# Kernel optimization log

Measured on AMD Instinct MI355X. Metric: run time of the kernel, lower is better.

Reference implementation:

```python
import jax, jax.numpy as jnp
import numpy as np

NUM_ANCHORS = 9


def select_tensor(tensor, inds):
    # tensor: (b, 9*c, h, w) -> rows (b*h*w*9, c), gather at inds (faithful to source layout)
    bs, c9, h, w = tensor.shape
    c = c9 // NUM_ANCHORS
    t = tensor.reshape(bs, NUM_ANCHORS, c, h * w).transpose(0, 3, 1, 2).reshape(-1, c)
    return t[inds]


def bilinear_sample(feat, bidx, ys, xs):
    # feat: (b, c, H, W); bidx/ys/xs: (P,). torchvision-style: 0 outside [-1, H]x[-1, W].
    H, W = feat.shape[2], feat.shape[3]
    invalid = (ys < -1.0) | (ys > H) | (xs < -1.0) | (xs > W)
    y = jnp.clip(ys, 0.0, H - 1)
    x = jnp.clip(xs, 0.0, W - 1)
    y0 = jnp.floor(y).astype(jnp.int32)
    x0 = jnp.floor(x).astype(jnp.int32)
    y1 = jnp.minimum(y0 + 1, H - 1)
    x1 = jnp.minimum(x0 + 1, W - 1)
    ly = (y - y0)[:, None]
    lx = (x - x0)[:, None]
    hy = 1.0 - ly
    hx = 1.0 - lx
    v00 = feat[bidx, :, y0, x0]
    v01 = feat[bidx, :, y0, x1]
    v10 = feat[bidx, :, y1, x0]
    v11 = feat[bidx, :, y1, x1]
    out = hy * hx * v00 + hy * lx * v01 + ly * hx * v10 + ly * lx * v11
    return jnp.where(invalid[:, None], 0.0, out)


def roi_align_3x3(feat, boxes, batch_idx):
    # output_size=(3,3), spatial_scale=1, sampling_ratio=1 (one center sample/bin), aligned=False
    OUT = 3
    n = boxes.shape[0]
    x1, y1, x2, y2 = boxes[:, 0], boxes[:, 1], boxes[:, 2], boxes[:, 3]
    roi_w = jnp.maximum(x2 - x1, 1.0)
    roi_h = jnp.maximum(y2 - y1, 1.0)
    bw = roi_w / OUT
    bh = roi_h / OUT
    g = jnp.arange(OUT, dtype=jnp.float32) + 0.5
    ys = jnp.broadcast_to(y1[:, None, None] + g[None, :, None] * bh[:, None, None], (n, OUT, OUT)).reshape(-1)
    xs = jnp.broadcast_to(x1[:, None, None] + g[None, None, :] * bw[:, None, None], (n, OUT, OUT)).reshape(-1)
    bidx = jnp.repeat(batch_idx, OUT * OUT)
    vals = bilinear_sample(feat, bidx, ys, xs)  # (n*9, c)
    return vals.reshape(n, OUT, OUT, feat.shape[1]).transpose(0, 3, 1, 2)  # (n, c, 3, 3)


def setup_inputs() -> dict:
    key = jax.random.key(0)
    ks = jax.random.split(key, 8)
    b, c, h, w = 8, 256, 128, 128
    return {
        "feat": jax.random.normal(ks[0], (b, c, h, w), dtype=jnp.float32),
        "hm": jax.random.uniform(ks[1], (b, 9, h, w), dtype=jnp.float32),
        "wh": jax.random.normal(ks[2], (b, 36, h, w), dtype=jnp.float32) * 4.0,
        "offset": jax.random.normal(ks[3], (b, 18, h, w), dtype=jnp.float32),
        "w_fc1": jax.random.normal(ks[4], (c * 9, 1024), dtype=jnp.float32) * 0.02,
        "b_fc1": jnp.zeros((1024,), dtype=jnp.float32),
        "w_cls": jax.random.normal(ks[5], (1024, 10), dtype=jnp.float32) * 0.02,
        "b_cls": jnp.zeros((10,), dtype=jnp.float32),
        "w_wh": jax.random.normal(ks[6], (1024, 4), dtype=jnp.float32) * 0.02,
        "b_wh": jnp.zeros((4,), dtype=jnp.float32),
        "k": 100,
    }


def reference(feat, hm, wh, offset, w_fc1, b_fc1, w_cls, b_cls, w_wh, b_wh, k):
    bs, _, h, w_ = hm.shape
    hw = h * w_
    # get_inds (inds=None path): topk over (b, h*w*9) with (h, w, anchor) flat layout
    flat = hm.transpose(0, 2, 3, 1).reshape(bs, -1)
    top_v, top_i = jax.lax.top_k(flat, k)
    value = top_v.reshape(-1)
    top_i = top_i.reshape(-1)
    stage1_cls = top_i % NUM_ANCHORS
    pos = (top_i // NUM_ANCHORS) % hw
    inds = pos + jnp.repeat(jnp.arange(bs, dtype=top_i.dtype) * hw, k)
    # select_tensor gathers (stage1 and for_stage2 use the same inds in the inference path)
    wh_sel = select_tensor(wh, inds)       # (b*k, 4)
    off_sel = select_tensor(offset, inds)  # (b*k, 2)
    # box arithmetic (faithful: ys = inds // w keeps the batch offset, as in the source)
    xs = (inds % w_).astype(jnp.float32) + off_sel[:, 0]
    ys = (inds // w_).astype(jnp.float32) + off_sel[:, 1]
    batch_idx = jnp.repeat(jnp.arange(bs), k)
    boxes = jnp.stack([xs + wh_sel[:, 0], ys + wh_sel[:, 1],
                       xs + wh_sel[:, 2], ys + wh_sel[:, 3]], axis=1)
    roi_feat = roi_align_3x3(feat, boxes, batch_idx)  # (b*k, c, 3, 3)
    # stage 2 head
    hdn = jax.nn.relu(roi_feat.reshape(roi_feat.shape[0], -1) @ w_fc1 + b_fc1)
    stage2_cls = hdn @ w_cls + b_cls
    stage2_wh = hdn @ w_wh + b_wh
    return (hm, wh_sel, off_sel, stage1_cls, wh_sel, off_sel, stage2_cls, stage2_wh, inds, value)
```

## Files before the change

### kernel.cpp

```cpp
#include <hip/hip_runtime.h>
#include <hip/hip_bf16.h>
#include <stdint.h>

#define HW      16384
#define W_      128
#define NA      9
#define BS      8
#define K_TOP   100
#define NDET    800
#define MPAD    832
#define C_FEAT  256
#define FC1_IN  2304
#define FC1_OUT 1024

#define O_HM    0
#define O_WH1   1179648
#define O_OFF1  1182848
#define O_S1CLS 1184448
#define O_WH2   1185248
#define O_OFF2  1188448
#define O_CLS   1190048
#define O_SWH   1198048
#define O_INDS  1201248
#define O_VAL   1202048

#define NBIN     1024
#define CAND_MAX 512
#define HBLK     36

typedef __attribute__((ext_vector_type(8))) short short8v;
typedef __attribute__((ext_vector_type(4))) float f32x4;

__device__ __forceinline__ void gload16(const void* g, void* l) {
    __builtin_amdgcn_global_load_lds(
        (const __attribute__((address_space(1))) unsigned int*)g,
        (__attribute__((address_space(3))) unsigned int*)l, 16, 0, 0);
}

__device__ __forceinline__ int binof(float v) {
    return max(0, min(NBIN - 1, (int)(v * (float)NBIN)));
}

__global__ __launch_bounds__(256) void hist_kernel(const float* __restrict__ hm,
                                                   float* __restrict__ out,
                                                   unsigned int* __restrict__ hist) {
    const int tid = threadIdx.x;
    const int b = blockIdx.x / HBLK, sub = blockIdx.x % HBLK;
    __shared__ unsigned int lh[NBIN];
    for (int i = tid; i < NBIN; i += 256) lh[i] = 0u;
    __syncthreads();
    const float4* src = (const float4*)(hm + (size_t)b * NA * HW) + sub * 1024;
    float4*       dst = (float4*)(out + O_HM + (size_t)b * NA * HW) + sub * 1024;
    #pragma unroll
    for (int t = 0; t < 4; ++t) {
        float4 v = src[t * 256 + tid];
        dst[t * 256 + tid] = v;
        atomicAdd(&lh[binof(v.x)], 1u);
        atomicAdd(&lh[binof(v.y)], 1u);
        atomicAdd(&lh[binof(v.z)], 1u);
        atomicAdd(&lh[binof(v.w)], 1u);
    }
    __syncthreads();
    for (int i = tid; i < NBIN; i += 256)
        if (lh[i]) atomicAdd(&hist[b * NBIN + i], lh[i]);
}

__global__ __launch_bounds__(512) void thresh_kernel(const unsigned int* __restrict__ hist,
                                                     int* __restrict__ thr) {
    const int b = threadIdx.x >> 6, lane = threadIdx.x & 63;
    const unsigned int* h = hist + b * NBIN;
    unsigned int s = 0;
    #pragma unroll
    for (int i = 0; i < 16; ++i) s += h[lane * 16 + i];
    unsigned int suf = s;
    #pragma unroll
    for (int off = 1; off < 64; off <<= 1) {
        unsigned int o = __shfl_down(suf, off);
        if (lane + off < 64) suf += o;
    }
    unsigned long long mask = __ballot(suf >= K_TOP);
    int L = 63 - __clzll(mask);
    unsigned int below = __shfl(suf, L + 1);
    if (L == 63) below = 0;
    if (lane == L) {
        unsigned int acc = below;
        int T = 16 * L;
        for (int i = 15; i >= 0; --i) {
            acc += h[16 * L + i];
            if (acc >= K_TOP) { T = 16 * L + i; break; }
        }
        thr[b] = T;
    }
}

__global__ __launch_bounds__(256) void collect_kernel(const float* __restrict__ hm,
                                                      const int* __restrict__ thr,
                                                      unsigned int* __restrict__ cnt,
                                                      unsigned long long* __restrict__ cand) {
    const int tid = threadIdx.x;
    const int b = blockIdx.x / HBLK, sub = blockIdx.x % HBLK;
    const int T = thr[b];
    const float4* src = (const float4*)(hm + (size_t)b * NA * HW) + sub * 1024;
    #pragma unroll
    for (int t = 0; t < 4; ++t) {
        int i4 = sub * 1024 + t * 256 + tid;
        float4 v4 = src[t * 256 + tid];
        float vv[4] = {v4.x, v4.y, v4.z, v4.w};
        #pragma unroll
        for (int e = 0; e < 4; ++e) {
            if (binof(vv[e]) >= T) {
                unsigned int p = atomicAdd(&cnt[b], 1u);
                if (p < CAND_MAX) {
                    int idx = i4 * 4 + e;
                    int a  = idx >> 14;
                    int pp = idx & (HW - 1);
                    unsigned int flat_i = (unsigned int)(pp * NA + a);
                    cand[b * CAND_MAX + p] =
                        ((unsigned long long)__float_as_uint(vv[e]) << 32)
                        | (unsigned long long)(0xFFFFFFFFu - flat_i);
                }
            }
        }
    }
}

__global__ __launch_bounds__(512) void sort_kernel(const unsigned long long* __restrict__ cand,
                                                   const unsigned int* __restrict__ cntg,
                                                   const float* __restrict__ wh,
                                                   const float* __restrict__ offset,
                                                   float* __restrict__ out,
                                                   float* __restrict__ ws_boxes) {
    const int b = blockIdx.x, tid = threadIdx.x;
    __shared__ unsigned long long cd[CAND_MAX];
    unsigned int cnt = cntg[b]; if (cnt > CAND_MAX) cnt = CAND_MAX;
    cd[tid] = (tid < (int)cnt) ? cand[b * CAND_MAX + tid] : 0ull;
    __syncthreads();
    for (int k = 2; k <= CAND_MAX; k <<= 1) {
        for (int j = k >> 1; j > 0; j >>= 1) {
            int i = tid, ixj = i ^ j;
            if (ixj > i) {
                unsigned long long a = cd[i], bb = cd[ixj];
                bool up = ((i & k) == 0);
                if (up ? (a < bb) : (a > bb)) { cd[i] = bb; cd[ixj] = a; }
            }
            __syncthreads();
        }
    }
    if (tid < K_TOP) {
        unsigned long long key = cd[tid];
        float v = __uint_as_float((unsigned int)(key >> 32));
        unsigned int flat_i = 0xFFFFFFFFu - (unsigned int)(key & 0xFFFFFFFFull);
        int a = (int)(flat_i % NA);
        int p = (int)(flat_i / NA);
        int inds = p + b * HW;
        int o = b * K_TOP + tid;
        out[O_VAL + o]   = v;
        out[O_S1CLS + o] = (float)a;
        out[O_INDS + o]  = (float)inds;
        int p2 = inds / NA;
        int a2 = inds - p2 * NA;
        float w0 = wh[(size_t)(a2 * 4 + 0) * HW + p2];
        float w1 = wh[(size_t)(a2 * 4 + 1) * HW + p2];
        float w2 = wh[(size_t)(a2 * 4 + 2) * HW + p2];
        float w3 = wh[(size_t)(a2 * 4 + 3) * HW + p2];
        float o0 = offset[(size_t)(a2 * 2 + 0) * HW + p2];
        float o1 = offset[(size_t)(a2 * 2 + 1) * HW + p2];
        out[O_WH1 + o * 4 + 0] = w0; out[O_WH1 + o * 4 + 1] = w1;
        out[O_WH1 + o * 4 + 2] = w2; out[O_WH1 + o * 4 + 3] = w3;
        out[O_WH2 + o * 4 + 0] = w0; out[O_WH2 + o * 4 + 1] = w1;
        out[O_WH2 + o * 4 + 2] = w2; out[O_WH2 + o * 4 + 3] = w3;
        out[O_OFF1 + o * 2 + 0] = o0; out[O_OFF1 + o * 2 + 1] = o1;
        out[O_OFF2 + o * 2 + 0] = o0; out[O_OFF2 + o * 2 + 1] = o1;
        float xs = (float)(inds % W_) + o0;
        float ys = (float)(inds / W_) + o1;
        ws_boxes[o * 4 + 0] = xs + w0;
        ws_boxes[o * 4 + 1] = ys + w1;
        ws_boxes[o * 4 + 2] = xs + w2;
        ws_boxes[o * 4 + 3] = ys + w3;
    }
}

__global__ __launch_bounds__(256) void roi_kernel(const float* __restrict__ feat,
                                                  const float* __restrict__ ws_boxes,
                                                  __hip_bfloat16* __restrict__ ws_roi) {
    int n = blockIdx.x;
    int c = threadIdx.x;
    __hip_bfloat16* op = ws_roi + (size_t)n * FC1_IN + (size_t)c * 9;
    if (n >= NDET) {
        #pragma unroll
        for (int i = 0; i < 9; ++i) op[i] = __float2bfloat16(0.0f);
        return;
    }
    float x1 = ws_boxes[n * 4 + 0], y1 = ws_boxes[n * 4 + 1];
    float x2 = ws_boxes[n * 4 + 2], y2 = ws_boxes[n * 4 + 3];
    int b = n / K_TOP;
    float bw = fmaxf(x2 - x1, 1.0f) / 3.0f;
    float bh = fmaxf(y2 - y1, 1.0f) / 3.0f;
    const float* fb = feat + ((size_t)b * C_FEAT + c) * HW;
    #pragma unroll
    for (int gy = 0; gy < 3; ++gy) {
        float ysf = y1 + ((float)gy + 0.5f) * bh;
        #pragma unroll
        for (int gx = 0; gx < 3; ++gx) {
            float xsf = x1 + ((float)gx + 0.5f) * bw;
            bool invalid = (ysf < -1.0f) || (ysf > 128.0f) || (xsf < -1.0f) || (xsf > 128.0f);
            float y = fminf(fmaxf(ysf, 0.0f), 127.0f);
            float x = fminf(fmaxf(xsf, 0.0f), 127.0f);
            int y0 = (int)floorf(y);
            int x0 = (int)floorf(x);
            int y1i = min(y0 + 1, 127);
            int x1i = min(x0 + 1, 127);
            float ly = y - (float)y0, lx = x - (float)x0;
            float hy = 1.0f - ly, hx = 1.0f - lx;
            float v00 = fb[y0 * W_ + x0],  v01 = fb[y0 * W_ + x1i];
            float v10 = fb[y1i * W_ + x0], v11 = fb[y1i * W_ + x1i];
            float v = hy * hx * v00 + hy * lx * v01 + ly * hx * v10 + ly * lx * v11;
            op[gy * 3 + gx] = __float2bfloat16(invalid ? 0.0f : v);
        }
    }
}

__global__ __launch_bounds__(256) void wt_kernel(const float* __restrict__ w,
                                                 __hip_bfloat16* __restrict__ wt) {
    __shared__ float t[64][65];
    int bk = blockIdx.x * 64;
    int bn = blockIdx.y * 64;
    int tid = threadIdx.x;
    int c = tid & 63, r = tid >> 6;
    for (int k = r; k < 64; k += 4)
        t[k][c] = w[(size_t)(bk + k) * FC1_OUT + bn + c];
    __syncthreads();
    for (int n = r; n < 64; n += 4)
        wt[(size_t)(bn + n) * FC1_IN + bk + c] = __float2bfloat16(t[c][n]);
}

__global__ __launch_bounds__(256) void fc1_mfma(const __hip_bfloat16* __restrict__ A,
                                                const __hip_bfloat16* __restrict__ WT,
                                                const float* __restrict__ bias,
                                                float* __restrict__ C) {
    __shared__ char smem[32768];
    const int tid = threadIdx.x;
    const int w = tid >> 6, l = tid & 63;
    const int bm0 = blockIdx.x * 64, bn0 = blockIdx.y * 64;
    const char* Ab = (const char*)A;
    const char* Bb = (const char*)WT;

    f32x4 acc[2][2];
    #pragma unroll
    for (int i = 0; i < 2; ++i)
        #pragma unroll
        for (int j = 0; j < 2; ++j) acc[i][j] = (f32x4){0.f, 0.f, 0.f, 0.f};

    const int wr = (w >> 1) * 32, wc = (w & 1) * 32;
    const int lrow = l & 15;
    const int lkb  = (l >> 4) * 16;

    auto STAGE = [&](int k0, int buf) {
        #pragma unroll
        for (int j = 0; j < 4; ++j) {
            int o = j * 4096 + tid * 16;
            const char* src;
            if (o < 8192) {
                int r = o >> 7, bby = o & 127;
                src = Ab + ((size_t)(bm0 + r) * FC1_IN + k0) * 2 + (bby ^ ((r & 7) << 4));
            } else {
                int o2 = o - 8192;
                int r = o2 >> 7, bby = o2 & 127;
                src = Bb + ((size_t)(bn0 + r) * FC1_IN + k0) * 2 + (bby ^ ((r & 7) << 4));
            }
            gload16(src, smem + buf * 16384 + o);
        }
    };

    STAGE(0, 0);
    __syncthreads();
    int cur = 0;
    #pragma unroll 1
    for (int t = 0; t < FC1_IN / 64; ++t) {
        if (t + 1 < FC1_IN / 64) STAGE((t + 1) * 64, cur ^ 1);
        char* sb = smem + cur * 16384;
        #pragma unroll
        for (int kk = 0; kk < 2; ++kk) {
            short8v af[2], bf[2];
            #pragma unroll
            for (int ms = 0; ms < 2; ++ms) {
                int r = wr + ms * 16 + lrow;
                int bby = kk * 64 + lkb;
                af[ms] = *(const short8v*)(sb + r * 128 + (bby ^ ((r & 7) << 4)));
            }
            #pragma unroll
            for (int ns = 0; ns < 2; ++ns) {
                int r = wc + ns * 16 + lrow;
                int bby = kk * 64 + lkb;
                bf[ns] = *(const short8v*)(sb + 8192 + r * 128 + (bby ^ ((r & 7) << 4)));
            }
            #pragma unroll
            for (int ms = 0; ms < 2; ++ms)
                #pragma unroll
                for (int ns = 0; ns < 2; ++ns)
                    acc[ms][ns] = __builtin_amdgcn_mfma_f32_16x16x32_bf16(
                        af[ms], bf[ns], acc[ms][ns], 0, 0, 0);
        }
        __syncthreads();
        cur ^= 1;
    }
    const int col = l & 15, rbase = (l >> 4) * 4;
    #pragma unroll
    for (int ms = 0; ms < 2; ++ms)
        #pragma unroll
        for (int ns = 0; ns < 2; ++ns)
            #pragma unroll
            for (int j = 0; j < 4; ++j) {
                int gm = bm0 + wr + ms * 16 + rbase + j;
                int gn = bn0 + wc + ns * 16 + col;
                if (gm < NDET)
                    C[(size_t)gm * FC1_OUT + gn] = fmaxf(acc[ms][ns][j] + bias[gn], 0.0f);
            }
}

__global__ __launch_bounds__(256) void fc2prep_kernel(const float* __restrict__ w_cls,
                                                      const float* __restrict__ w_wh,
                                                      float* __restrict__ wT14) {
    int idx = blockIdx.x * 256 + threadIdx.x;
    int j = idx >> 10, k = idx & 1023;
    wT14[idx] = (j < 10) ? w_cls[k * 10 + j] : w_wh[k * 4 + (j - 10)];
}

__global__ __launch_bounds__(256) void fc2_kernel(const float* __restrict__ hdn,
                                                  const float* __restrict__ wT14,
                                                  const float* __restrict__ b_cls,
                                                  const float* __restrict__ b_wh,
                                                  float* __restrict__ out) {
    int n = blockIdx.x;
    int lane = threadIdx.x & 63, wv = threadIdx.x >> 6;
    const float4* h4 = (const float4*)(hdn + (size_t)n * FC1_OUT);
    for (int j = wv; j < 14; j += 4) {
        const float4* w4 = (const float4*)(wT14 + (size_t)j * FC1_OUT);
        float s = 0.0f;
        #pragma unroll
        for (int t = 0; t < 4; ++t) {
            float4 a = h4[t * 64 + lane], b = w4[t * 64 + lane];
            s += a.x * b.x + a.y * b.y + a.z * b.z + a.w * b.w;
        }
        #pragma unroll
        for (int off = 32; off > 0; off >>= 1) s += __shfl_down(s, off);
        if (lane == 0) {
            if (j < 10) out[O_CLS + n * 10 + j] = s + b_cls[j];
            else        out[O_SWH + n * 4 + (j - 10)] = s + b_wh[j - 10];
        }
    }
}

extern "C" void kernel_launch(void* const* d_in, const int* in_sizes, int n_in,
                              void* d_out, int out_size, void* d_ws, size_t ws_size,
                              hipStream_t stream) {
    const float* feat   = (const float*)d_in[0];
    const float* hm     = (const float*)d_in[1];
    const float* wh     = (const float*)d_in[2];
    const float* offset = (const float*)d_in[3];
    const float* w_fc1  = (const float*)d_in[4];
    const float* b_fc1  = (const float*)d_in[5];
    const float* w_cls  = (const float*)d_in[6];
    const float* b_cls  = (const float*)d_in[7];
    const float* w_wh   = (const float*)d_in[8];
    const float* b_wh   = (const float*)d_in[9];
    float* out = (float*)d_out;

    char* ws = (char*)d_ws;
    float*              ws_boxes = (float*)(ws + 4096);
    unsigned int*       ws_hist  = (unsigned int*)(ws + 20480);
    unsigned int*       ws_cnt   = (unsigned int*)(ws + 53248);
    int*                ws_thr   = (int*)(ws + 53280);
    unsigned long long* ws_cand  = (unsigned long long*)(ws + 57344);
    __hip_bfloat16*     ws_wt    = (__hip_bfloat16*)(ws + 98304);
    __hip_bfloat16*     ws_roi   = (__hip_bfloat16*)(ws + 98304 + 4718592);
    float*              ws_hdn   = (float*)(ws + 98304 + 4718592 + 3833856);
    float*              ws_wT14  = (float*)(ws + 98304 + 4718592 + 3833856 + 3276800);

    hipMemsetAsync(ws + 20480, 0, 32832, stream);

    hist_kernel   <<<BS * HBLK, 256, 0, stream>>>(hm, out, ws_hist);
    thresh_kernel <<<1, 512, 0, stream>>>(ws_hist, ws_thr);
    collect_kernel<<<BS * HBLK, 256, 0, stream>>>(hm, ws_thr, ws_cnt, ws_cand);
    sort_kernel   <<<BS, 512, 0, stream>>>(ws_cand, ws_cnt, wh, offset, out, ws_boxes);
    wt_kernel     <<<dim3(FC1_IN / 64, FC1_OUT / 64), 256, 0, stream>>>(w_fc1, ws_wt);
    roi_kernel    <<<MPAD, 256, 0, stream>>>(feat, ws_boxes, ws_roi);
    fc1_mfma      <<<dim3(MPAD / 64, FC1_OUT / 64), 256, 0, stream>>>(ws_roi, ws_wt, b_fc1, ws_hdn);
    fc2prep_kernel<<<56, 256, 0, stream>>>(w_cls, w_wh, ws_wT14);
    fc2_kernel    <<<NDET, 256, 0, stream>>>(ws_hdn, ws_wT14, b_cls, b_wh, out);
}
```

Baseline: 288.8 us.

## Fuse top-k, weight prep and ROI align into one cooperative kernel

Merges the histogram, threshold, candidate collection, sort, weight transposes and ROI align stages into one cooperative kernel that uses grid-wide syncs instead of separate launches. The heatmap slice is kept in LDS so the collect pass does not re-read it from global memory. Per-block histograms are written out and reduced after a grid sync, which removes the global atomics and the memset. The bitonic sort now uses all threads on both halves, and fc2 caches its weights in LDS while processing 8 rows per block. The cost is three grid syncs over only 256 blocks, and each of those blocks holds a large LDS footprint.

After: 381.3 us. 32.0% more time.

```diff
diff --git a/kernel.cpp b/kernel.cpp
--- a/kernel.cpp
+++ b/kernel.cpp
@@ -1,6 +1,9 @@
 #include <hip/hip_runtime.h>
 #include <hip/hip_bf16.h>
+#include <hip/hip_cooperative_groups.h>
 #include <stdint.h>
+
+namespace cg = cooperative_groups;
 
 #define HW      16384
 #define W_      128
@@ -26,7 +29,6 @@
 
 #define NBIN     1024
 #define CAND_MAX 512
-#define HBLK     36
 
 typedef __attribute__((ext_vector_type(8))) short short8v;
 typedef __attribute__((ext_vector_type(4))) float f32x4;
@@ -41,197 +43,215 @@
     return max(0, min(NBIN - 1, (int)(v * (float)NBIN)));
 }
 
-__global__ __launch_bounds__(256) void hist_kernel(const float* __restrict__ hm,
-                                                   float* __restrict__ out,
-                                                   unsigned int* __restrict__ hist) {
-    const int tid = threadIdx.x;
-    const int b = blockIdx.x / HBLK, sub = blockIdx.x % HBLK;
-    __shared__ unsigned int lh[NBIN];
-    for (int i = tid; i < NBIN; i += 256) lh[i] = 0u;
+struct CoopArgs {
+    const float* hm; const float* feat; const float* wh; const float* offset;
+    const float* w_fc1; const float* w_cls; const float* w_wh;
+    float* out; unsigned int* histp; unsigned int* cnt;
+    unsigned long long* cand; float* boxes;
+    __hip_bfloat16* wt; float* wT14; __hip_bfloat16* roi;
+};
+
+__global__ __launch_bounds__(256) void coop_kernel(CoopArgs a) {
+    __shared__ float4 slice[1152];
+    __shared__ unsigned int lhist[NBIN];
+    __shared__ float wtt[64][65];
+    __shared__ unsigned long long cd[CAND_MAX];
+    __shared__ int s_T;
+
+    cg::grid_group grid = cg::this_grid();
+    const int bid = blockIdx.x, tid = threadIdx.x;
+    const int batch = bid >> 5, sub = bid & 31;
+
+    for (int i = tid; i < NBIN; i += 256) lhist[i] = 0u;
+    if (bid < BS && tid == 0) a.cnt[bid] = 0u;
     __syncthreads();
-    const float4* src = (const float4*)(hm + (size_t)b * NA * HW) + sub * 1024;
-    float4*       dst = (float4*)(out + O_HM + (size_t)b * NA * HW) + sub * 1024;
-    #pragma unroll
-    for (int t = 0; t < 4; ++t) {
-        float4 v = src[t * 256 + tid];
-        dst[t * 256 + tid] = v;
-        atomicAdd(&lh[binof(v.x)], 1u);
-        atomicAdd(&lh[binof(v.y)], 1u);
-        atomicAdd(&lh[binof(v.z)], 1u);
-        atomicAdd(&lh[binof(v.w)], 1u);
+
+    {
+        const float4* src = (const float4*)(a.hm + (size_t)batch * NA * HW) + sub * 1152;
+        float4*       dst = (float4*)(a.out + O_HM + (size_t)batch * NA * HW) + sub * 1152;
+        for (int i = tid; i < 1152; i += 256) {
+            float4 v = src[i];
+            dst[i] = v;
+            slice[i] = v;
+            atomicAdd(&lhist[binof(v.x)], 1u);
+            atomicAdd(&lhist[binof(v.y)], 1u);
+            atomicAdd(&lhist[binof(v.z)], 1u);
+            atomicAdd(&lhist[binof(v.w)], 1u);
+        }
+        __syncthreads();
+        for (int i = tid; i < NBIN; i += 256) a.histp[bid * NBIN + i] = lhist[i];
+    }
+
+    {
+        const int c = tid & 63, r = tid >> 6;
+        for (int t = bid; t < 576; t += 256) {
+            int bk = (t % 36) * 64, bn = (t / 36) * 64;
+            for (int k = r; k < 64; k += 4)
+                wtt[k][c] = a.w_fc1[(size_t)(bk + k) * FC1_OUT + bn + c];
+            __syncthreads();
+            for (int nn = r; nn < 64; nn += 4)
+                a.wt[(size_t)(bn + nn) * FC1_IN + bk + c] = __float2bfloat16(wtt[c][nn]);
+            __syncthreads();
+        }
+    }
+    if (bid < 56) {
+        int idx = bid * 256 + tid;
+        int j = idx >> 10, k = idx & 1023;
+        a.wT14[idx] = (j < 10) ? a.w_cls[k * 10 + j] : a.w_wh[k * 4 + (j - 10)];
+    }
+
+    grid.sync();
+
+    for (int i = tid; i < NBIN; i += 256) {
+        unsigned int s = 0;
+        #pragma unroll 8
+        for (int sb = 0; sb < 32; ++sb) s += a.histp[(size_t)(batch * 32 + sb) * NBIN + i];
+        lhist[i] = s;
     }
     __syncthreads();
-    for (int i = tid; i < NBIN; i += 256)
-        if (lh[i]) atomicAdd(&hist[b * NBIN + i], lh[i]);
-}
-
-__global__ __launch_bounds__(512) void thresh_kernel(const unsigned int* __restrict__ hist,
-                                                     int* __restrict__ thr) {
-    const int b = threadIdx.x >> 6, lane = threadIdx.x & 63;
-    const unsigned int* h = hist + b * NBIN;
-    unsigned int s = 0;
-    #pragma unroll
-    for (int i = 0; i < 16; ++i) s += h[lane * 16 + i];
-    unsigned int suf = s;
-    #pragma unroll
-    for (int off = 1; off < 64; off <<= 1) {
-        unsigned int o = __shfl_down(suf, off);
-        if (lane + off < 64) suf += o;
-    }
-    unsigned long long mask = __ballot(suf >= K_TOP);
-    int L = 63 - __clzll(mask);
-    unsigned int below = __shfl(suf, L + 1);
-    if (L == 63) below = 0;
-    if (lane == L) {
-        unsigned int acc = below;
-        int T = 16 * L;
-        for (int i = 15; i >= 0; --i) {
-            acc += h[16 * L + i];
-            if (acc >= K_TOP) { T = 16 * L + i; break; }
-        }
-        thr[b] = T;
-    }
-}
-
-__global__ __launch_bounds__(256) void collect_kernel(const float* __restrict__ hm,
-                                                      const int* __restrict__ thr,
-                                                      unsigned int* __restrict__ cnt,
-                                                      unsigned long long* __restrict__ cand) {
-    const int tid = threadIdx.x;
-    const int b = blockIdx.x / HBLK, sub = blockIdx.x % HBLK;
-    const int T = thr[b];
-    const float4* src = (const float4*)(hm + (size_t)b * NA * HW) + sub * 1024;
-    #pragma unroll
-    for (int t = 0; t < 4; ++t) {
-        int i4 = sub * 1024 + t * 256 + tid;
-        float4 v4 = src[t * 256 + tid];
-        float vv[4] = {v4.x, v4.y, v4.z, v4.w};
-        #pragma unroll
-        for (int e = 0; e < 4; ++e) {
-            if (binof(vv[e]) >= T) {
-                unsigned int p = atomicAdd(&cnt[b], 1u);
-                if (p < CAND_MAX) {
-                    int idx = i4 * 4 + e;
-                    int a  = idx >> 14;
-                    int pp = idx & (HW - 1);
-                    unsigned int flat_i = (unsigned int)(pp * NA + a);
-                    cand[b * CAND_MAX + p] =
-                        ((unsigned long long)__float_as_uint(vv[e]) << 32)
-                        | (unsigned long long)(0xFFFFFFFFu - flat_i);
+    if (tid < 64) {
+        int lane = tid;
+        unsigned int s = 0;
+        #pragma unroll
+        for (int i = 0; i < 16; ++i) s += lhist[lane * 16 + i];
+        unsigned int suf = s;
+        #pragma unroll
+        for (int off = 1; off < 64; off <<= 1) {
+            unsigned int o = __shfl_down(suf, off);
+            if (lane + off < 64) suf += o;
+        }
+        unsigned long long mask = __ballot(suf >= K_TOP);
+        int L = 63 - __clzll(mask);
+        unsigned int below = __shfl(suf, L + 1);
+        if (L == 63) below = 0;
+        if (lane == L) {
+            unsigned int acc = below;
+            int T = 16 * L;
+            for (int i = 15; i >= 0; --i) {
+                acc += lhist[16 * L + i];
+                if (acc >= K_TOP) { T = 16 * L + i; break; }
+            }
+            s_T = T;
+        }
+    }
+    __syncthreads();
+    {
+        const int T = s_T;
+        for (int i = tid; i < 1152; i += 256) {
+            float4 v4 = slice[i];
+            float vv[4] = {v4.x, v4.y, v4.z, v4.w};
+            #pragma unroll
+            for (int e = 0; e < 4; ++e) {
+                if (binof(vv[e]) >= T) {
+                    unsigned int p = atomicAdd(&a.cnt[batch], 1u);
+                    if (p < CAND_MAX) {
+                        int idx = (sub * 1152 + i) * 4 + e;
+                        int an = idx >> 14;
+                        int pp = idx & (HW - 1);
+                        unsigned int flat_i = (unsigned int)(pp * NA + an);
+                        a.cand[batch * CAND_MAX + p] =
+                            ((unsigned long long)__float_as_uint(vv[e]) << 32)
+                            | (unsigned long long)(0xFFFFFFFFu - flat_i);
+                    }
                 }
             }
         }
     }
-}
-
-__global__ __launch_bounds__(512) void sort_kernel(const unsigned long long* __restrict__ cand,
-                                                   const unsigned int* __restrict__ cntg,
-                                                   const float* __restrict__ wh,
-                                                   const float* __restrict__ offset,
-                                                   float* __restrict__ out,
-                                                   float* __restrict__ ws_boxes) {
-    const int b = blockIdx.x, tid = threadIdx.x;
-    __shared__ unsigned long long cd[CAND_MAX];
-    unsigned int cnt = cntg[b]; if (cnt > CAND_MAX) cnt = CAND_MAX;
-    cd[tid] = (tid < (int)cnt) ? cand[b * CAND_MAX + tid] : 0ull;
-    __syncthreads();
-    for (int k = 2; k <= CAND_MAX; k <<= 1) {
-        for (int j = k >> 1; j > 0; j >>= 1) {
-            int i = tid, ixj = i ^ j;
-            if (ixj > i) {
-                unsigned long long a = cd[i], bb = cd[ixj];
+
+    grid.sync();
+
+    if (bid < BS) {
+        const int b = bid;
+        unsigned int c = a.cnt[b]; if (c > CAND_MAX) c = CAND_MAX;
+        cd[tid]       = (tid < (int)c)       ? a.cand[b * CAND_MAX + tid]       : 0ull;
+        cd[tid + 256] = (tid + 256 < (int)c) ? a.cand[b * CAND_MAX + tid + 256] : 0ull;
+        __syncthreads();
+        for (int k = 2; k <= CAND_MAX; k <<= 1) {
+            for (int j = k >> 1; j > 0; j >>= 1) {
+                int i   = ((tid & ~(j - 1)) << 1) | (tid & (j - 1));
+                int ixj = i | j;
+                unsigned long long x = cd[i], y = cd[ixj];
                 bool up = ((i & k) == 0);
-                if (up ? (a < bb) : (a > bb)) { cd[i] = bb; cd[ixj] = a; }
-            }
-            __syncthreads();
-        }
-    }
-    if (tid < K_TOP) {
-        unsigned long long key = cd[tid];
-        float v = __uint_as_float((unsigned int)(key >> 32));
-        unsigned int flat_i = 0xFFFFFFFFu - (unsigned int)(key & 0xFFFFFFFFull);
-        int a = (int)(flat_i % NA);
-        int p = (int)(flat_i / NA);
-        int inds = p + b * HW;
-        int o = b * K_TOP + tid;
-        out[O_VAL + o]   = v;
-        out[O_S1CLS + o] = (float)a;
-        out[O_INDS + o]  = (float)inds;
-        int p2 = inds / NA;
-        int a2 = inds - p2 * NA;
-        float w0 = wh[(size_t)(a2 * 4 + 0) * HW + p2];
-        float w1 = wh[(size_t)(a2 * 4 + 1) * HW + p2];
-        float w2 = wh[(size_t)(a2 * 4 + 2) * HW + p2];
-        float w3 = wh[(size_t)(a2 * 4 + 3) * HW + p2];
-        float o0 = offset[(size_t)(a2 * 2 + 0) * HW + p2];
-        float o1 = offset[(size_t)(a2 * 2 + 1) * HW + p2];
-        out[O_WH1 + o * 4 + 0] = w0; out[O_WH1 + o * 4 + 1] = w1;
-        out[O_WH1 + o * 4 + 2] = w2; out[O_WH1 + o * 4 + 3] = w3;
-        out[O_WH2 + o * 4 + 0] = w0; out[O_WH2 + o * 4 + 1] = w1;
-        out[O_WH2 + o * 4 + 2] = w2; out[O_WH2 + o * 4 + 3] = w3;
-        out[O_OFF1 + o * 2 + 0] = o0; out[O_OFF1 + o * 2 + 1] = o1;
-        out[O_OFF2 + o * 2 + 0] = o0; out[O_OFF2 + o * 2 + 1] = o1;
-        float xs = (float)(inds % W_) + o0;
-        float ys = (float)(inds / W_) + o1;
-        ws_boxes[o * 4 + 0] = xs + w0;
-        ws_boxes[o * 4 + 1] = ys + w1;
-        ws_boxes[o * 4 + 2] = xs + w2;
-        ws_boxes[o * 4 + 3] = ys + w3;
-    }
-}
-
-__global__ __launch_bounds__(256) void roi_kernel(const float* __restrict__ feat,
-                                                  const float* __restrict__ ws_boxes,
-                                                  __hip_bfloat16* __restrict__ ws_roi) {
-    int n = blockIdx.x;
-    int c = threadIdx.x;
-    __hip_bfloat16* op = ws_roi + (size_t)n * FC1_IN + (size_t)c * 9;
-    if (n >= NDET) {
-        #pragma unroll
-        for (int i = 0; i < 9; ++i) op[i] = __float2bfloat16(0.0f);
-        return;
-    }
-    float x1 = ws_boxes[n * 4 + 0], y1 = ws_boxes[n * 4 + 1];
-    float x2 = ws_boxes[n * 4 + 2], y2 = ws_boxes[n * 4 + 3];
-    int b = n / K_TOP;
-    float bw = fmaxf(x2 - x1, 1.0f) / 3.0f;
-    float bh = fmaxf(y2 - y1, 1.0f) / 3.0f;
-    const float* fb = feat + ((size_t)b * C_FEAT + c) * HW;
-    #pragma unroll
-    for (int gy = 0; gy < 3; ++gy) {
-        float ysf = y1 + ((float)gy + 0.5f) * bh;
-        #pragma unroll
-        for (int gx = 0; gx < 3; ++gx) {
-            float xsf = x1 + ((float)gx + 0.5f) * bw;
-            bool invalid = (ysf < -1.0f) || (ysf > 128.0f) || (xsf < -1.0f) || (xsf > 128.0f);
-            float y = fminf(fmaxf(ysf, 0.0f), 127.0f);
-            float x = fminf(fmaxf(xsf, 0.0f), 127.0f);
-            int y0 = (int)floorf(y);
-            int x0 = (int)floorf(x);
-            int y1i = min(y0 + 1, 127);
-            int x1i = min(x0 + 1, 127);
-            float ly = y - (float)y0, lx = x - (float)x0;
-            float hy = 1.0f - ly, hx = 1.0f - lx;
-            float v00 = fb[y0 * W_ + x0],  v01 = fb[y0 * W_ + x1i];
-            float v10 = fb[y1i * W_ + x0], v11 = fb[y1i * W_ + x1i];
-            float v = hy * hx * v00 + hy * lx * v01 + ly * hx * v10 + ly * lx * v11;
-            op[gy * 3 + gx] = __float2bfloat16(invalid ? 0.0f : v);
-        }
-    }
-}
-
-__global__ __launch_bounds__(256) void wt_kernel(const float* __restrict__ w,
-                                                 __hip_bfloat16* __restrict__ wt) {
-    __shared__ float t[64][65];
-    int bk = blockIdx.x * 64;
-    int bn = blockIdx.y * 64;
-    int tid = threadIdx.x;
-    int c = tid & 63, r = tid >> 6;
-    for (int k = r; k < 64; k += 4)
-        t[k][c] = w[(size_t)(bk + k) * FC1_OUT + bn + c];
-    __syncthreads();
-    for (int n = r; n < 64; n += 4)
-        wt[(size_t)(bn + n) * FC1_IN + bk + c] = __float2bfloat16(t[c][n]);
+                if (up ? (x < y) : (x > y)) { cd[i] = y; cd[ixj] = x; }
+                __syncthreads();
+            }
+        }
+        if (tid < K_TOP) {
+            unsigned long long key = cd[tid];
+            float v = __uint_as_float((unsigned int)(key >> 32));
+            unsigned int flat_i = 0xFFFFFFFFu - (unsigned int)(key & 0xFFFFFFFFull);
+            int an = (int)(flat_i % NA);
+            int p  = (int)(flat_i / NA);
+            int inds = p + b * HW;
+            int o = b * K_TOP + tid;
+            a.out[O_VAL + o]   = v;
+            a.out[O_S1CLS + o] = (float)an;
+            a.out[O_INDS + o]  = (float)inds;
+            int p2 = inds / NA;
+            int a2 = inds - p2 * NA;
+            float w0 = a.wh[(size_t)(a2 * 4 + 0) * HW + p2];
+            float w1 = a.wh[(size_t)(a2 * 4 + 1) * HW + p2];
+            float w2 = a.wh[(size_t)(a2 * 4 + 2) * HW + p2];
+            float w3 = a.wh[(size_t)(a2 * 4 + 3) * HW + p2];
+            float o0 = a.offset[(size_t)(a2 * 2 + 0) * HW + p2];
+            float o1 = a.offset[(size_t)(a2 * 2 + 1) * HW + p2];
+            a.out[O_WH1 + o * 4 + 0] = w0; a.out[O_WH1 + o * 4 + 1] = w1;
+            a.out[O_WH1 + o * 4 + 2] = w2; a.out[O_WH1 + o * 4 + 3] = w3;
+            a.out[O_WH2 + o * 4 + 0] = w0; a.out[O_WH2 + o * 4 + 1] = w1;
+            a.out[O_WH2 + o * 4 + 2] = w2; a.out[O_WH2 + o * 4 + 3] = w3;
+            a.out[O_OFF1 + o * 2 + 0] = o0; a.out[O_OFF1 + o * 2 + 1] = o1;
+            a.out[O_OFF2 + o * 2 + 0] = o0; a.out[O_OFF2 + o * 2 + 1] = o1;
+            float xs = (float)(inds % W_) + o0;
+            float ys = (float)(inds / W_) + o1;
+            a.boxes[o * 4 + 0] = xs + w0;
+            a.boxes[o * 4 + 1] = ys + w1;
+            a.boxes[o * 4 + 2] = xs + w2;
+            a.boxes[o * 4 + 3] = ys + w3;
+        }
+    }
+
+    grid.sync();
+
+    for (int n = bid; n < MPAD; n += 256) {
+        const int c = tid;
+        __hip_bfloat16* op = a.roi + (size_t)n * FC1_IN + (size_t)c * 9;
+        if (n >= NDET) {
+            #pragma unroll
+            for (int i = 0; i < 9; ++i) op[i] = __float2bfloat16(0.0f);
+            continue;
+        }
+        float x1 = a.boxes[n * 4 + 0], y1 = a.boxes[n * 4 + 1];
+        float x2 = a.boxes[n * 4 + 2], y2 = a.boxes[n * 4 + 3];
+        int b = n / K_TOP;
+        float bw = fmaxf(x2 - x1, 1.0f) / 3.0f;
+        float bh = fmaxf(y2 - y1, 1.0f) / 3.0f;
+        const float* fb = a.feat + ((size_t)b * C_FEAT + c) * HW;
+        #pragma unroll
+        for (int gy = 0; gy < 3; ++gy) {
+            float ysf = y1 + ((float)gy + 0.5f) * bh;
+            #pragma unroll
+            for (int gx = 0; gx < 3; ++gx) {
+                float xsf = x1 + ((float)gx + 0.5f) * bw;
+                bool invalid = (ysf < -1.0f) || (ysf > 128.0f) || (xsf < -1.0f) || (xsf > 128.0f);
+                if (invalid) {
+                    op[gy * 3 + gx] = __float2bfloat16(0.0f);
+                    continue;
+                }
+                float y = fminf(fmaxf(ysf, 0.0f), 127.0f);
+                float x = fminf(fmaxf(xsf, 0.0f), 127.0f);
+                int y0 = (int)floorf(y);
+                int x0 = (int)floorf(x);
+                int y1i = min(y0 + 1, 127);
+                int x1i = min(x0 + 1, 127);
+                float ly = y - (float)y0, lx = x - (float)x0;
+                float hy = 1.0f - ly, hx = 1.0f - lx;
+                float v00 = fb[y0 * W_ + x0],  v01 = fb[y0 * W_ + x1i];
+                float v10 = fb[y1i * W_ + x0], v11 = fb[y1i * W_ + x1i];
+                float v = hy * hx * v00 + hy * lx * v01 + ly * hx * v10 + ly * lx * v11;
+                op[gy * 3 + gx] = __float2bfloat16(v);
+            }
+        }
+    }
 }
 
 __global__ __launch_bounds__(256) void fc1_mfma(const __hip_bfloat16* __restrict__ A,
@@ -318,35 +338,39 @@
             }
 }
 
-__global__ __launch_bounds__(256) void fc2prep_kernel(const float* __restrict__ w_cls,
-                                                      const float* __restrict__ w_wh,
-                                                      float* __restrict__ wT14) {
-    int idx = blockIdx.x * 256 + threadIdx.x;
-    int j = idx >> 10, k = idx & 1023;
-    wT14[idx] = (j < 10) ? w_cls[k * 10 + j] : w_wh[k * 4 + (j - 10)];
-}
-
 __global__ __launch_bounds__(256) void fc2_kernel(const float* __restrict__ hdn,
                                                   const float* __restrict__ wT14,
                                                   const float* __restrict__ b_cls,
                                                   const float* __restrict__ b_wh,
                                                   float* __restrict__ out) {
-    int n = blockIdx.x;
-    int lane = threadIdx.x & 63, wv = threadIdx.x >> 6;
-    const float4* h4 = (const float4*)(hdn + (size_t)n * FC1_OUT);
-    for (int j = wv; j < 14; j += 4) {
-        const float4* w4 = (const float4*)(wT14 + (size_t)j * FC1_OUT);
-        float s = 0.0f;
-        #pragma unroll
-        for (int t = 0; t < 4; ++t) {
-            float4 a = h4[t * 64 + lane], b = w4[t * 64 + lane];
-            s += a.x * b.x + a.y * b.y + a.z * b.z + a.w * b.w;
-        }
-        #pragma unroll
-        for (int off = 32; off > 0; off >>= 1) s += __shfl_down(s, off);
-        if (lane == 0) {
-            if (j < 10) out[O_CLS + n * 10 + j] = s + b_cls[j];
-            else        out[O_SWH + n * 4 + (j - 10)] = s + b_wh[j - 10];
+    __shared__ float4 wl4[3584];
+    __shared__ float bl[14];
+    const int tid = threadIdx.x;
+    const float4* wg4 = (const float4*)wT14;
+    for (int i = tid; i < 3584; i += 256) wl4[i] = wg4[i];
+    if (tid < 14) bl[tid] = (tid < 10) ? b_cls[tid] : b_wh[tid - 10];
+    __syncthreads();
+    const int wv = tid >> 6, lane = tid & 63;
+    #pragma unroll
+    for (int pass = 0; pass < 2; ++pass) {
+        int n = blockIdx.x * 8 + pass * 4 + wv;
+        const float4* h4 = (const float4*)(hdn + (size_t)n * FC1_OUT);
+        float4 hr[4];
+        #pragma unroll
+        for (int t = 0; t < 4; ++t) hr[t] = h4[t * 64 + lane];
+        for (int j = 0; j < 14; ++j) {
+            float s = 0.0f;
+            #pragma unroll
+            for (int t = 0; t < 4; ++t) {
+                float4 w = wl4[j * 256 + t * 64 + lane];
+                s += hr[t].x * w.x + hr[t].y * w.y + hr[t].z * w.z + hr[t].w * w.w;
+            }
+            #pragma unroll
+            for (int off = 32; off > 0; off >>= 1) s += __shfl_down(s, off);
+            if (lane == 0) {
+                if (j < 10) out[O_CLS + n * 10 + j] = s + bl[j];
+                else        out[O_SWH + n * 4 + (j - 10)] = s + bl[j];
+            }
         }
     }
 }
@@ -367,25 +391,25 @@
     float* out = (float*)d_out;
 
     char* ws = (char*)d_ws;
-    float*              ws_boxes = (float*)(ws + 4096);
-    unsigned int*       ws_hist  = (unsigned int*)(ws + 20480);
-    unsigned int*       ws_cnt   = (unsigned int*)(ws + 53248);
-    int*                ws_thr   = (int*)(ws + 53280);
-    unsigned long long* ws_cand  = (unsigned long long*)(ws + 57344);
-    __hip_bfloat16*     ws_wt    = (__hip_bfloat16*)(ws + 98304);
-    __hip_bfloat16*     ws_roi   = (__hip_bfloat16*)(ws + 98304 + 4718592);
-    float*              ws_hdn   = (float*)(ws + 98304 + 4718592 + 3833856);
-    float*              ws_wT14  = (float*)(ws + 98304 + 4718592 + 3833856 + 3276800);
-
-    hipMemsetAsync(ws + 20480, 0, 32832, stream);
-
-    hist_kernel   <<<BS * HBLK, 256, 0, stream>>>(hm, out, ws_hist);
-    thresh_kernel <<<1, 512, 0, stream>>>(ws_hist, ws_thr);
-    collect_kernel<<<BS * HBLK, 256, 0, stream>>>(hm, ws_thr, ws_cnt, ws_cand);
-    sort_kernel   <<<BS, 512, 0, stream>>>(ws_cand, ws_cnt, wh, offset, out, ws_boxes);
-    wt_kernel     <<<dim3(FC1_IN / 64, FC1_OUT / 64), 256, 0, stream>>>(w_fc1, ws_wt);
-    roi_kernel    <<<MPAD, 256, 0, stream>>>(feat, ws_boxes, ws_roi);
-    fc1_mfma      <<<dim3(MPAD / 64, FC1_OUT / 64), 256, 0, stream>>>(ws_roi, ws_wt, b_fc1, ws_hdn);
-    fc2prep_kernel<<<56, 256, 0, stream>>>(w_cls, w_wh, ws_wT14);
-    fc2_kernel    <<<NDET, 256, 0, stream>>>(ws_hdn, ws_wT14, b_cls, b_wh, out);
-}
+    float*              ws_boxes = (float*)(ws + 0);
+    unsigned int*       ws_cnt   = (unsigned int*)(ws + 16384);
+    unsigned long long* ws_cand  = (unsigned long long*)(ws + 32768);
+    unsigned int*       ws_histp = (unsigned int*)(ws + 65536);
+    float*              ws_wT14  = (float*)(ws + 1114112);
+    __hip_bfloat16*     ws_wt    = (__hip_bfloat16*)(ws + 1171456);
+    __hip_bfloat16*     ws_roi   = (__hip_bfloat16*)(ws + 5890048);
+    float*              ws_hdn   = (float*)(ws + 9723904);
+
+    CoopArgs ca;
+    ca.hm = hm; ca.feat = feat; ca.wh = wh; ca.offset = offset;
+    ca.w_fc1 = w_fc1; ca.w_cls = w_cls; ca.w_wh = w_wh;
+    ca.out = out; ca.histp = ws_histp; ca.cnt = ws_cnt;
+    ca.cand = ws_cand; ca.boxes = ws_boxes;
+    ca.wt = ws_wt; ca.wT14 = ws_wT14; ca.roi = ws_roi;
+
+    void* kargs[] = { &ca };
+    hipLaunchCooperativeKernel((void*)coop_kernel, dim3(256), dim3(256), kargs, 0, stream);
+
+    fc1_mfma  <<<dim3(MPAD / 64, FC1_OUT / 64), 256, 0, stream>>>(ws_roi, ws_wt, b_fc1, ws_hdn);
+    fc2_kernel<<<NDET / 8, 256, 0, stream>>>(ws_hdn, ws_wT14, b_cls, b_wh, out);
+}
```
